# Kernel optimization log

Hardware: AMD Instinct MI355X
Metric: run time of the kernel (lower is better)

Reference implementation:

```python
import jax, jax.numpy as jnp
import numpy as np

HID = 3584
NH = 28
NKV = 4
HD = HID // NH  # 128
T = 2048
THETA = 1000000.0
SCALE = HD ** -0.5


def setup_inputs() -> dict:
    key = jax.random.key(0)
    ks = jax.random.split(key, 9)
    s = 0.02
    return {
        "positions": jnp.arange(T, dtype=jnp.int32),
        "hidden_states": jax.random.normal(ks[0], (T, HID), dtype=jnp.float32),
        "wq": jax.random.normal(ks[1], (HID, NH * HD), dtype=jnp.float32) * s,
        "bq": jax.random.normal(ks[2], (NH * HD,), dtype=jnp.float32) * s,
        "wk": jax.random.normal(ks[3], (HID, NKV * HD), dtype=jnp.float32) * s,
        "bk": jax.random.normal(ks[4], (NKV * HD,), dtype=jnp.float32) * s,
        "wv": jax.random.normal(ks[5], (HID, NKV * HD), dtype=jnp.float32) * s,
        "bv": jax.random.normal(ks[6], (NKV * HD,), dtype=jnp.float32) * s,
        "wo": jax.random.normal(ks[7], (NH * HD, HID), dtype=jnp.float32) * s,
    }


def _rope(x, positions):
    # neox-style RoPE over full head_dim: split halves, rotate.
    half = HD // 2
    inv_freq = 1.0 / (THETA ** (jnp.arange(0, half, dtype=jnp.float32) / half))
    ang = positions.astype(jnp.float32)[:, None] * inv_freq  # [T, half]
    cos = jnp.cos(ang)[:, None, :]  # [T, 1, half]
    sin = jnp.sin(ang)[:, None, :]
    x1, x2 = x[..., :half], x[..., half:]
    return jnp.concatenate([x1 * cos - x2 * sin, x2 * cos + x1 * sin], axis=-1)


def reference(positions, hidden_states, wq, bq, wk, bk, wv, bv, wo):
    q = (hidden_states @ wq + bq).reshape(T, NH, HD)
    k = (hidden_states @ wk + bk).reshape(T, NKV, HD)
    v = (hidden_states @ wv + bv).reshape(T, NKV, HD)
    q = _rope(q, positions)
    k = _rope(k, positions)
    # GQA: expand kv heads to query heads (groups of NH//NKV)
    g = NH // NKV
    k = jnp.repeat(k, g, axis=1)  # [T, NH, HD]
    v = jnp.repeat(v, g, axis=1)
    scores = jnp.einsum("thd,shd->hts", q, k) * SCALE  # bidirectional, no mask
    probs = jax.nn.softmax(scores, axis=-1)
    attn = jnp.einsum("hts,shd->thd", probs, v).reshape(T, NH * HD)
    return attn @ wo
```

## Files before the change

### kernel.cpp

```cpp
#include <hip/hip_runtime.h>

typedef __bf16 bf16_t;
typedef __attribute__((ext_vector_type(8))) __bf16 bf16x8;
typedef __attribute__((ext_vector_type(4))) float floatx4;

#define T_SEQ 2048
#define HID 3584
#define NH 28
#define NKV 4
#define HD 128
#define GQA 7
#define SCALE_F 0.08838834764831845f
#define QSCALE_LOG2 0.1275179100693744f

__global__ void conv_bf_k(const float* __restrict__ src, bf16_t* __restrict__ dst, long n) {
  const long i = ((long)blockIdx.x * 256 + threadIdx.x) * 8;
  if (i >= n) return;
  const floatx4 a = *(const floatx4*)(src + i);
  const floatx4 b = *(const floatx4*)(src + i + 4);
  bf16x8 r;
  r[0] = (bf16_t)a[0]; r[1] = (bf16_t)a[1]; r[2] = (bf16_t)a[2]; r[3] = (bf16_t)a[3];
  r[4] = (bf16_t)b[0]; r[5] = (bf16_t)b[1]; r[6] = (bf16_t)b[2]; r[7] = (bf16_t)b[3];
  *(bf16x8*)(dst + i) = r;
}

__global__ __launch_bounds__(256) void tconv_k(const float* __restrict__ src,
                                               bf16_t* __restrict__ dst, long N, long K) {
  __shared__ alignas(16) bf16_t t[64][72];
  const long k0 = (long)blockIdx.y * 64, n0 = (long)blockIdx.x * 64;
  const int tid = threadIdx.x;
  const int rr = tid >> 4;
  const int cc = (tid & 15) * 4;
#pragma unroll
  for (int i = 0; i < 4; ++i) {
    const int r = rr + i * 16;
    const floatx4 v = *(const floatx4*)(src + (k0 + r) * N + n0 + cc);
#pragma unroll
    for (int j = 0; j < 4; ++j) t[cc + j][r] = (bf16_t)v[j];
  }
  __syncthreads();
#pragma unroll
  for (int i = 0; i < 2; ++i) {
    const int J = i * 256 + tid;
    const int n = J >> 3, c8 = (J & 7) * 8;
    *(bf16x8*)(dst + (n0 + n) * K + k0 + c8) = *(const bf16x8*)(&t[n][c8]);
  }
}

__device__ __forceinline__ bf16x8 ld8(const void* p, long idx, bool f32) {
  if (f32) {
    const float* q = (const float*)p + idx;
    const floatx4 u = *(const floatx4*)q;
    const floatx4 v = *(const floatx4*)(q + 4);
    bf16x8 r;
    r[0] = (bf16_t)u[0]; r[1] = (bf16_t)u[1]; r[2] = (bf16_t)u[2]; r[3] = (bf16_t)u[3];
    r[4] = (bf16_t)v[0]; r[5] = (bf16_t)v[1]; r[6] = (bf16_t)v[2]; r[7] = (bf16_t)v[3];
    return r;
  }
  return *(const bf16x8*)((const bf16_t*)p + idx);
}

__device__ __forceinline__ void gld16(const bf16_t* g, bf16_t* l) {
  __builtin_amdgcn_global_load_lds(
      (const __attribute__((address_space(1))) unsigned int*)(const void*)g,
      (__attribute__((address_space(3))) unsigned int*)(void*)l, 16, 0, 0);
}

__global__ __launch_bounds__(256) void gemm_bt_k(
    const bf16_t* __restrict__ A, long lda,
    const bf16_t* __restrict__ Bt, long ldb,
    const float* __restrict__ bias, void* Cv, long ldc,
    int K, int mode, void* Cv2) {
  __shared__ alignas(16) bf16_t ldsA[128 * 32];
  __shared__ alignas(16) bf16_t ldsB[128 * 32];
  const int tid = threadIdx.x;
  const int lane = tid & 63;
  const int w = tid >> 6;
  const int wr = w >> 1, wc = w & 1;
  const int col = lane & 15, quad = lane >> 4;

  const int nwg = gridDim.x * gridDim.y;
  const int bid = blockIdx.y * gridDim.x + blockIdx.x;
  const int cpx = nwg >> 3;
  const int lb = (bid & 7) * cpx + (bid >> 3);
  const long m0 = (long)(lb / gridDim.x) * 128, n0 = (long)(lb % gridDim.x) * 128;

  const int r0 = tid >> 2;
  const int c0 = tid & 3;
  const int cs = c0 ^ ((r0 >> 1) & 3);
  const int r1 = 64 + r0;

  floatx4 acc[4][4] = {};

  for (int k0 = 0; k0 < K; k0 += 32) {
    gld16(A + (m0 + r0) * lda + k0 + cs * 8, ldsA + tid * 8);
    gld16(A + (m0 + r1) * lda + k0 + cs * 8, ldsA + (256 + tid) * 8);
    gld16(Bt + (n0 + r0) * ldb + k0 + cs * 8, ldsB + tid * 8);
    gld16(Bt + (n0 + r1) * ldb + k0 + cs * 8, ldsB + (256 + tid) * 8);
    __syncthreads();
    bf16x8 af[4], bf[4];
#pragma unroll
    for (int i = 0; i < 4; ++i) {
      const int ra = wr * 64 + i * 16 + col;
      af[i] = *(const bf16x8*)(ldsA + ra * 32 + (quad ^ ((ra >> 1) & 3)) * 8);
    }
#pragma unroll
    for (int j = 0; j < 4; ++j) {
      const int rb = wc * 64 + j * 16 + col;
      bf[j] = *(const bf16x8*)(ldsB + rb * 32 + (quad ^ ((rb >> 1) & 3)) * 8);
    }
#pragma unroll
    for (int i = 0; i < 4; ++i)
#pragma unroll
      for (int j = 0; j < 4; ++j)
        acc[i][j] = __builtin_amdgcn_mfma_f32_16x16x32_bf16(af[i], bf[j], acc[i][j], 0, 0, 0);
    __syncthreads();
  }

#pragma unroll
  for (int i = 0; i < 4; ++i) {
#pragma unroll
    for (int j = 0; j < 4; ++j) {
      const long row0 = m0 + wr * 64 + i * 16 + quad * 4;
      const long cc = n0 + wc * 64 + j * 16 + col;
      const float bvv = bias ? bias[cc] : 0.f;
#pragma unroll
      for (int r = 0; r < 4; ++r) {
        const float v = acc[i][j][r] + bvv;
        if (mode == 0)      ((bf16_t*)Cv)[(row0 + r) * ldc + cc] = (bf16_t)v;
        else if (mode == 1) ((float*)Cv)[(row0 + r) * ldc + cc] = v;
        else {
          if (cc < 3584)      ((bf16_t*)Cv)[(row0 + r) * ldc + cc] = (bf16_t)v;
          else if (cc < 4096) ((bf16_t*)Cv2)[(row0 + r) * 512 + (cc - 3584)] = (bf16_t)v;
          else ((bf16_t*)Cv2)[1048576 + (cc - 4096) * (long)T_SEQ + (row0 + r)] = (bf16_t)v;
        }
      }
    }
  }
}

__global__ __launch_bounds__(256) void gemm_nt_k(
    const void* A, long lda, const void* B, long ldb,
    const float* bias, void* Cv, long ldc,
    int K, int aMode, int bMode, int transC, int c32, const int* flag) {
  __shared__ alignas(16) bf16_t ldsA[128 * 32];
  __shared__ alignas(16) unsigned int ldsB32[128 * 16];
  const int f = *flag;
  const bool aF32 = aMode && (f > 32);
  const bool bF32 = bMode && (f > 32);
  const int tid = threadIdx.x;
  const int lane = tid & 63;
  const int w = tid >> 6;
  const int wr = w >> 1, wc = w & 1;
  const int col = lane & 15, quad = lane >> 4;
  const long m0 = (long)blockIdx.y * 128, n0 = (long)blockIdx.x * 128;

  const int ar1 = tid >> 2, ak = (tid & 3) * 8;
  const int ar2 = 64 + ar1;
  const int kk = (tid >> 4) * 2;
  const int nn = (tid & 15) * 8;
  const int kp = kk >> 1;

  floatx4 acc[4][4] = {};

  for (int k0 = 0; k0 < K; k0 += 32) {
    const bf16x8 a1 = ld8(A, (m0 + ar1) * lda + k0 + ak, aF32);
    const bf16x8 a2 = ld8(A, (m0 + ar2) * lda + k0 + ak, aF32);
    const bf16x8 b0 = ld8(B, (long)(k0 + kk) * ldb + n0 + nn, bF32);
    const bf16x8 b1 = ld8(B, (long)(k0 + kk + 1) * ldb + n0 + nn, bF32);
    __syncthreads();
    *(bf16x8*)(ldsA + ar1 * 32 + ak) = a1;
    *(bf16x8*)(ldsA + ar2 * 32 + ak) = a2;
#pragma unroll
    for (int j = 0; j < 8; ++j) {
      const int n = nn + j;
      const int pk = ((((kp >> 2) ^ ((n >> 3) & 3)) << 2) | (kp & 3));
      union { struct { bf16_t lo, hi; } s; unsigned int u; } cv;
      cv.s.lo = b0[j];
      cv.s.hi = b1[j];
      ldsB32[n * 16 + pk] = cv.u;
    }
    __syncthreads();
    bf16x8 af[4], bfv[4];
#pragma unroll
    for (int i = 0; i < 4; ++i)
      af[i] = *(const bf16x8*)(ldsA + (wr * 64 + i * 16 + col) * 32 + quad * 8);
#pragma unroll
    for (int j = 0; j < 4; ++j) {
      const int n = wc * 64 + j * 16 + col;
      const int blk = quad ^ ((n >> 3) & 3);
      bfv[j] = *(const bf16x8*)((const bf16_t*)(ldsB32 + n * 16 + blk * 4));
    }
#pragma unroll
    for (int i = 0; i < 4; ++i)
#pragma unroll
      for (int jj = 0; jj < 4; ++jj)
        acc[i][jj] = __builtin_amdgcn_mfma_f32_16x16x32_bf16(af[i], bfv[jj], acc[i][jj], 0, 0, 0);
  }

#pragma unroll
  for (int i = 0; i < 4; ++i) {
#pragma unroll
    for (int j = 0; j < 4; ++j) {
      const long row0 = m0 + wr * 64 + i * 16 + quad * 4;
      const long cc = n0 + wc * 64 + j * 16 + col;
      const float bvv = bias ? bias[cc] : 0.f;
#pragma unroll
      for (int r = 0; r < 4; ++r) {
        const float v = acc[i][j][r] + bvv;
        if (transC)   ((bf16_t*)Cv)[cc * ldc + (row0 + r)] = (bf16_t)v;
        else if (c32) ((float*)Cv)[(row0 + r) * ldc + cc] = v;
        else          ((bf16_t*)Cv)[(row0 + r) * ldc + cc] = (bf16_t)v;
      }
    }
  }
}

__global__ void rope_k(bf16_t* buf, const int* __restrict__ pos, long ld, int nheads) {
  const int idx = blockIdx.x * 256 + threadIdx.x;
  const int total = T_SEQ * nheads * 64;
  if (idx >= total) return;
  const int d = idx & 63;
  const int th = idx >> 6;
  const int h = th % nheads;
  const int t = th / nheads;
  const float inv = exp2f((float)d * (-19.931568569324174f / 64.f));
  const float ang = (float)pos[t] * inv;
  float sn, cs;
  __sincosf(ang, &sn, &cs);
  bf16_t* p = buf + (long)t * ld + h * HD + d;
  const float x1 = (float)p[0];
  const float x2 = (float)p[64];
  p[0] = (bf16_t)(x1 * cs - x2 * sn);
  p[64] = (bf16_t)(x2 * cs + x1 * sn);
}

__global__ __launch_bounds__(256, 2) void attn5_k(
    const bf16_t* __restrict__ q, long qs,
    const bf16_t* __restrict__ k, long ks,
    const bf16_t* __restrict__ vt,
    bf16_t* __restrict__ out, long os) {
  __shared__ alignas(16) bf16_t ldsK[2][64 * 128];
  __shared__ alignas(16) bf16_t ldsV[2][128 * 64];
  __shared__ alignas(16) bf16_t pbuf[4][32 * 64];

  const int h = blockIdx.y;
  const long hkvHD = (long)(h / GQA) * HD;
  const int tid = threadIdx.x;
  const int lane = tid & 63;
  const int w = tid >> 6;
  const int col = lane & 15, quad = lane >> 4;
  const int t0 = blockIdx.x * 128 + w * 32;

  auto stage = [&](int buf, int t) {
    const long s0 = (long)t * 64;
#pragma unroll
    for (int i = 0; i < 4; ++i) {
      const int J = i * 256 + tid;
      {
        const int row = J >> 4;
        const int cs = (J & 15) ^ (row & 7);
        gld16(k + (s0 + row) * ks + hkvHD + cs * 8, &ldsK[buf][J * 8]);
      }
      {
        const int row = J >> 3;
        const int cs = (J & 7) ^ (row & 7);
        gld16(vt + (hkvHD + row) * T_SEQ + s0 + cs * 8, &ldsV[buf][J * 8]);
      }
    }
  };

  bf16x8 aq[2][4];
#pragma unroll
  for (int sub = 0; sub < 2; ++sub) {
    const bf16_t* qp = q + (long)(t0 + sub * 16 + col) * qs + h * HD + quad * 8;
#pragma unroll
    for (int c = 0; c < 4; ++c) {
      aq[sub][c] = *(const bf16x8*)(qp + c * 32);
#pragma unroll
      for (int e = 0; e < 8; ++e)
        aq[sub][c][e] = (bf16_t)((float)aq[sub][c][e] * QSCALE_LOG2);
    }
  }

  bf16x8 ones;
#pragma unroll
  for (int e = 0; e < 8; ++e) ones[e] = (bf16_t)1.0f;

  floatx4 O[2][8] = {};
  float m_w[2] = {-1e30f, -1e30f};
  float l_i[2][4] = {};

  stage(0, 0);
  for (int t = 0; t < 32; ++t) {
    const int cur = t & 1;
    stage(cur ^ 1, (t + 1) & 31);
    __builtin_amdgcn_sched_barrier(0);
    asm volatile("s_waitcnt vmcnt(8)" ::: "memory");
    __builtin_amdgcn_sched_barrier(0);
    __builtin_amdgcn_s_barrier();
    __builtin_amdgcn_sched_barrier(0);

    floatx4 S[2][4] = {};
    __builtin_amdgcn_s_setprio(1);
#pragma unroll
    for (int nt = 0; nt < 4; ++nt) {
      const int row = nt * 16 + col;
#pragma unroll
      for (int c = 0; c < 4; ++c) {
        const int cs = (c * 4 + quad) ^ (row & 7);
        const bf16x8 bk = *(const bf16x8*)(&ldsK[cur][row * 128 + cs * 8]);
        S[0][nt] = __builtin_amdgcn_mfma_f32_16x16x32_bf16(aq[0][c], bk, S[0][nt], 0, 0, 0);
        S[1][nt] = __builtin_amdgcn_mfma_f32_16x16x32_bf16(aq[1][c], bk, S[1][nt], 0, 0, 0);
      }
    }
    __builtin_amdgcn_s_setprio(0);

#pragma unroll
    for (int sub = 0; sub < 2; ++sub) {
      float mx = S[sub][0][0];
#pragma unroll
      for (int nt = 0; nt < 4; ++nt)
#pragma unroll
        for (int r = 0; r < 4; ++r) mx = fmaxf(mx, S[sub][nt][r]);
#pragma unroll
      for (int off = 1; off < 64; off <<= 1)
        mx = fmaxf(mx, __shfl_xor(mx, off, 64));
      if (mx > m_w[sub] + 12.0f) {
        const float alpha = exp2f(m_w[sub] - mx);
        m_w[sub] = mx;
#pragma unroll
        for (int r = 0; r < 4; ++r) l_i[sub][r] *= alpha;
#pragma unroll
        for (int dt = 0; dt < 8; ++dt)
#pragma unroll
          for (int r = 0; r < 4; ++r) O[sub][dt][r] *= alpha;
      }
    }

#pragma unroll
    for (int sub = 0; sub < 2; ++sub)
#pragma unroll
      for (int r = 0; r < 4; ++r) {
        const int mrow = sub * 16 + quad * 4 + r;
#pragma unroll
        for (int nt = 0; nt < 4; ++nt) {
          const float p = exp2f(S[sub][nt][r] - m_w[sub]);
          const int cs = (nt * 2 + (col >> 3)) ^ (mrow & 7);
          pbuf[w][mrow * 64 + cs * 8 + (col & 7)] = (bf16_t)p;
        }
      }

    floatx4 Ssum[2] = {};
    __builtin_amdgcn_s_setprio(1);
#pragma unroll
    for (int kb = 0; kb < 2; ++kb) {
      const int csp = (kb * 4 + quad) ^ (col & 7);
      const bf16x8 pa0 = *(const bf16x8*)(&pbuf[w][(col) * 64 + csp * 8]);
      const bf16x8 pa1 = *(const bf16x8*)(&pbuf[w][(16 + col) * 64 + csp * 8]);
      Ssum[0] = __builtin_amdgcn_mfma_f32_16x16x32_bf16(pa0, ones, Ssum[0], 0, 0, 0);
      Ssum[1] = __builtin_amdgcn_mfma_f32_16x16x32_bf16(pa1, ones, Ssum[1], 0, 0, 0);
#pragma unroll
      for (int dt = 0; dt < 8; ++dt) {
        const int vrow = dt * 16 + col;
        const bf16x8 bv = *(const bf16x8*)(&ldsV[cur][vrow * 64 + csp * 8]);
        O[0][dt] = __builtin_amdgcn_mfma_f32_16x16x32_bf16(pa0, bv, O[0][dt], 0, 0, 0);
        O[1][dt] = __builtin_amdgcn_mfma_f32_16x16x32_bf16(pa1, bv, O[1][dt], 0, 0, 0);
      }
    }
    __builtin_amdgcn_s_setprio(0);
#pragma unroll
    for (int sub = 0; sub < 2; ++sub)
#pragma unroll
      for (int r = 0; r < 4; ++r) l_i[sub][r] += Ssum[sub][r];

    __builtin_amdgcn_sched_barrier(0);
    __builtin_amdgcn_s_barrier();
    __builtin_amdgcn_sched_barrier(0);
  }

#pragma unroll
  for (int sub = 0; sub < 2; ++sub) {
#pragma unroll
    for (int r = 0; r < 4; ++r) l_i[sub][r] = 1.f / l_i[sub][r];
#pragma unroll
    for (int dt = 0; dt < 8; ++dt) {
#pragma unroll
      for (int r = 0; r < 4; ++r) {
        const long trow = t0 + sub * 16 + quad * 4 + r;
        out[trow * os + h * HD + dt * 16 + col] = (bf16_t)(O[sub][dt][r] * l_i[sub][r]);
      }
    }
  }
}

extern "C" void kernel_launch(void* const* d_in, const int* in_sizes, int n_in,
                              void* d_out_v, int out_size, void* d_ws, size_t ws_size,
                              hipStream_t stream) {
  const int* pos = (const int*)d_in[0];
  const float* hidden = (const float*)d_in[1];
  const float* wq = (const float*)d_in[2];
  const float* bq = (const float*)d_in[3];
  const float* wk = (const float*)d_in[4];
  const float* bk = (const float*)d_in[5];
  const float* wv = (const float*)d_in[6];
  const float* bv = (const float*)d_in[7];
  const float* wo = (const float*)d_in[8];

  bf16_t* qbuf = (bf16_t*)d_out_v;
  bf16_t* attn_hi = (bf16_t*)d_out_v + (size_t)T_SEQ * HID;
  float* outf = (float*)d_out_v;

  char* ws = (char*)d_ws;
  const size_t NEED = 51904516;

  if (ws_size >= NEED) {
    bf16_t* hbf  = (bf16_t*)ws;
    bf16_t* wqbt = (bf16_t*)(ws + 14680064);
    bf16_t* wkbt = (bf16_t*)(ws + 40370176);
    bf16_t* wvbt = (bf16_t*)(ws + 44040192);
    bf16_t* kbuf = (bf16_t*)(ws + 47710208);
    bf16_t* vt   = (bf16_t*)(ws + 49807360);
    bf16_t* wobt = wqbt;
    bf16_t* attnb = hbf;
    float* bqkv = (float*)attn_hi;

    hipMemcpyAsync(bqkv, bq, 3584 * sizeof(float), hipMemcpyDeviceToDevice, stream);
    hipMemcpyAsync(bqkv + 3584, bk, 512 * sizeof(float), hipMemcpyDeviceToDevice, stream);
    hipMemcpyAsync(bqkv + 4096, bv, 512 * sizeof(float), hipMemcpyDeviceToDevice, stream);

    conv_bf_k<<<3584, 256, 0, stream>>>(hidden, hbf, (long)T_SEQ * HID);
    tconv_k<<<dim3(56, 56), 256, 0, stream>>>(wq, wqbt, HID, HID);
    tconv_k<<<dim3(8, 56), 256, 0, stream>>>(wk, wkbt, 512, HID);
    tconv_k<<<dim3(8, 56), 256, 0, stream>>>(wv, wvbt, 512, HID);

    gemm_bt_k<<<dim3(36, 16), 256, 0, stream>>>(hbf, HID, wqbt, HID, bqkv, qbuf, HID,
                                                HID, 3, kbuf);

    rope_k<<<(T_SEQ * NH * 64) / 256, 256, 0, stream>>>(qbuf, pos, HID, NH);
    rope_k<<<(T_SEQ * NKV * 64) / 256, 256, 0, stream>>>(kbuf, pos, 512, NKV);

    attn5_k<<<dim3(16, 28), 256, 0, stream>>>(qbuf, HID, kbuf, 512, vt, attnb, HID);

    tconv_k<<<dim3(56, 56), 256, 0, stream>>>(wo, wobt, HID, HID);

    gemm_bt_k<<<dim3(28, 16), 256, 0, stream>>>(attnb, HID, wobt, HID, nullptr,
                                                outf, HID, HID, 1, nullptr);
  } else {
    bf16_t* kbuf = (bf16_t*)ws;
    bf16_t* vt = (bf16_t*)(ws + 2097152);
    bf16_t* acopy = (bf16_t*)ws;
    int* flag = (int*)(ws + 4194304);

    hipMemsetAsync(flag, 64, 4, stream);

    gemm_nt_k<<<dim3(28, 16), 256, 0, stream>>>(hidden, HID, wq, HID, bq, qbuf, HID,
                                                HID, 1, 1, 0, 0, flag);
    gemm_nt_k<<<dim3(4, 16), 256, 0, stream>>>(hidden, HID, wk, 512, bk, kbuf, 512,
                                               HID, 1, 1, 0, 0, flag);
    gemm_nt_k<<<dim3(4, 16), 256, 0, stream>>>(hidden, HID, wv, 512, bv, vt, T_SEQ,
                                               HID, 1, 1, 1, 0, flag);

    rope_k<<<(T_SEQ * NH * 64) / 256, 256, 0, stream>>>(qbuf, pos, HID, NH);
    rope_k<<<(T_SEQ * NKV * 64) / 256, 256, 0, stream>>>(kbuf, pos, 512, NKV);

    attn5_k<<<dim3(16, 28), 256, 0, stream>>>(qbuf, HID, kbuf, 512, vt, attn_hi, HID);

    hipMemcpyAsync(acopy, attn_hi + (size_t)1536 * HID, (size_t)512 * HID * 2,
                   hipMemcpyDeviceToDevice, stream);
    gemm_nt_k<<<dim3(28, 8), 256, 0, stream>>>(attn_hi, HID, wo, HID, nullptr,
                                               outf, HID, HID, 0, 1, 0, 1, flag);
    gemm_nt_k<<<dim3(28, 4), 256, 0, stream>>>(attn_hi + (size_t)1024 * HID, HID, wo, HID,
                                               nullptr, outf + (size_t)1024 * HID, HID,
                                               HID, 0, 1, 0, 1, flag);
    gemm_nt_k<<<dim3(28, 4), 256, 0, stream>>>(acopy, HID, wo, HID,
                                               nullptr, outf + (size_t)1536 * HID, HID,
                                               HID, 0, 1, 0, 1, flag);
  }
}
```

Measured before the change: 524.5 us.

## Double-buffer GEMM LDS tiles and prefetch next K-tile during MFMA

The bf16 GEMM kernel now keeps two LDS buffers and issues the global-to-LDS loads for the next K tile before computing on the current one. It waits with a partial vmcnt so that only the current tile's loads must have landed. This hides global memory latency behind the MFMA work. The change also drops the XCD-aware block remapping in favour of plain blockIdx ordering, which may reduce L2 locality. The last iteration issues a redundant reload of tile 0, and the kernel's LDS use doubles, which can lower occupancy.

```diff
diff --git a/kernel.cpp b/kernel.cpp
--- a/kernel.cpp
+++ b/kernel.cpp
@@ -71,50 +71,62 @@
     const bf16_t* __restrict__ Bt, long ldb,
     const float* __restrict__ bias, void* Cv, long ldc,
     int K, int mode, void* Cv2) {
-  __shared__ alignas(16) bf16_t ldsA[128 * 32];
-  __shared__ alignas(16) bf16_t ldsB[128 * 32];
+  __shared__ alignas(16) bf16_t ldsA[2][128 * 32];
+  __shared__ alignas(16) bf16_t ldsB[2][128 * 32];
   const int tid = threadIdx.x;
   const int lane = tid & 63;
   const int w = tid >> 6;
   const int wr = w >> 1, wc = w & 1;
   const int col = lane & 15, quad = lane >> 4;
-
-  const int nwg = gridDim.x * gridDim.y;
-  const int bid = blockIdx.y * gridDim.x + blockIdx.x;
-  const int cpx = nwg >> 3;
-  const int lb = (bid & 7) * cpx + (bid >> 3);
-  const long m0 = (long)(lb / gridDim.x) * 128, n0 = (long)(lb % gridDim.x) * 128;
+  const long m0 = (long)blockIdx.y * 128, n0 = (long)blockIdx.x * 128;
 
   const int r0 = tid >> 2;
   const int c0 = tid & 3;
   const int cs = c0 ^ ((r0 >> 1) & 3);
   const int r1 = 64 + r0;
 
+  const bf16_t* Ab = A + m0 * lda + cs * 8;
+  const bf16_t* Bb = Bt + n0 * ldb + cs * 8;
+
   floatx4 acc[4][4] = {};
-
-  for (int k0 = 0; k0 < K; k0 += 32) {
-    gld16(A + (m0 + r0) * lda + k0 + cs * 8, ldsA + tid * 8);
-    gld16(A + (m0 + r1) * lda + k0 + cs * 8, ldsA + (256 + tid) * 8);
-    gld16(Bt + (n0 + r0) * ldb + k0 + cs * 8, ldsB + tid * 8);
-    gld16(Bt + (n0 + r1) * ldb + k0 + cs * 8, ldsB + (256 + tid) * 8);
-    __syncthreads();
+  const int nt = K >> 5;
+
+  auto stage = [&](int buf, int t) {
+    const long k0 = (long)t << 5;
+    gld16(Ab + (long)r0 * lda + k0, ldsA[buf] + tid * 8);
+    gld16(Ab + (long)r1 * lda + k0, ldsA[buf] + (256 + tid) * 8);
+    gld16(Bb + (long)r0 * ldb + k0, ldsB[buf] + tid * 8);
+    gld16(Bb + (long)r1 * ldb + k0, ldsB[buf] + (256 + tid) * 8);
+  };
+
+  stage(0, 0);
+  for (int t = 0; t < nt; ++t) {
+    const int cur = t & 1;
+    stage(cur ^ 1, (t + 1 == nt) ? 0 : t + 1);
+    __builtin_amdgcn_sched_barrier(0);
+    asm volatile("s_waitcnt vmcnt(4)" ::: "memory");
+    __builtin_amdgcn_sched_barrier(0);
+    __builtin_amdgcn_s_barrier();
+    __builtin_amdgcn_sched_barrier(0);
     bf16x8 af[4], bf[4];
 #pragma unroll
     for (int i = 0; i < 4; ++i) {
       const int ra = wr * 64 + i * 16 + col;
-      af[i] = *(const bf16x8*)(ldsA + ra * 32 + (quad ^ ((ra >> 1) & 3)) * 8);
+      af[i] = *(const bf16x8*)(ldsA[cur] + ra * 32 + (quad ^ ((ra >> 1) & 3)) * 8);
     }
 #pragma unroll
     for (int j = 0; j < 4; ++j) {
       const int rb = wc * 64 + j * 16 + col;
-      bf[j] = *(const bf16x8*)(ldsB + rb * 32 + (quad ^ ((rb >> 1) & 3)) * 8);
+      bf[j] = *(const bf16x8*)(ldsB[cur] + rb * 32 + (quad ^ ((rb >> 1) & 3)) * 8);
     }
 #pragma unroll
     for (int i = 0; i < 4; ++i)
 #pragma unroll
       for (int j = 0; j < 4; ++j)
         acc[i][j] = __builtin_amdgcn_mfma_f32_16x16x32_bf16(af[i], bf[j], acc[i][j], 0, 0, 0);
-    __syncthreads();
+    __builtin_amdgcn_sched_barrier(0);
+    __builtin_amdgcn_s_barrier();
+    __builtin_amdgcn_sched_barrier(0);
   }
 
 #pragma unroll
```

Result: faster. 502.6 us (-4.2%).
